# Kernel optimization log

Hardware: AMD Instinct MI355X
Metric: run time of the kernel (lower is better)

## Reference

```python
import jax, jax.numpy as jnp
import numpy as np

EPS_Q = 1e-5
EPS_RMS = 1e-6


def _bitlinear(x, w):
    # absmean ternary weight quantization with STE (STE irrelevant for fwd)
    w_scale = jnp.maximum(jnp.mean(jnp.abs(w)), EPS_Q)
    w_q = jnp.clip(jnp.round(w / w_scale), -1.0, 1.0)
    w_q = jax.lax.stop_gradient(w_q - w) + w
    # per-token absmax activation quantization
    x_scale = jnp.maximum(jnp.max(jnp.abs(x), axis=-1, keepdims=True), EPS_Q)
    x_s = x / x_scale
    out = jnp.einsum('bi,oi->bo', x_s, w_q)
    return out * x_scale


def _rmsnorm(x, g):
    rms = jnp.sqrt(jnp.mean(x * x, axis=-1, keepdims=True) + EPS_RMS)
    return x / rms * g


def setup_inputs() -> dict:
    key = jax.random.key(0)
    ks = jax.random.split(key, 6)
    B, IN, H, OUT = 65536, 784, 1024, 10
    return {
        'x': jax.random.normal(ks[0], (B, IN), dtype=jnp.float32),
        'w1': jax.random.normal(ks[1], (H, IN), dtype=jnp.float32) * 0.02,
        'g1': jnp.ones((H,), dtype=jnp.float32),
        'w2': jax.random.normal(ks[2], (H, H), dtype=jnp.float32) * 0.02,
        'g2': jnp.ones((H,), dtype=jnp.float32),
        'w3': jax.random.normal(ks[3], (OUT, H), dtype=jnp.float32) * 0.02,
    }


def reference(x, w1, g1, w2, g2, w3):
    h = _bitlinear(x, w1)
    h = jax.nn.gelu(_rmsnorm(h, g1), approximate=False)
    h = _bitlinear(h, w2)
    h = jax.nn.gelu(_rmsnorm(h, g2), approximate=False)
    return _bitlinear(h, w3)
```

## Files before the change

### kernel.cpp

```cpp
#include <hip/hip_runtime.h>
#include <hip/hip_bf16.h>
#include <stdint.h>


typedef __attribute__((ext_vector_type(8))) short short8;
typedef __attribute__((ext_vector_type(4))) float f32x4;

#define B_TOTAL 65536
#define IN_DIM 784
#define IN_PAD 832
#define H_DIM 1024
#define OUT_DIM 10
#define OUT_PAD 16

__device__ __forceinline__ unsigned short f2bf(float f) {
    union { float f; unsigned u; } c; c.f = f;
    unsigned r = c.u + 0x7FFFu + ((c.u >> 16) & 1u);
    return (unsigned short)(r >> 16);
}
__device__ __forceinline__ float bf2f(unsigned short h) {
    union { unsigned u; float f; } c; c.u = ((unsigned)h) << 16;
    return c.f;
}

__device__ __forceinline__ float gelu_fast(float t) {
    const float z = t * 0.70710678118f;
    const float s = fabsf(z);
    const float tt = 1.0f / (1.0f + 0.3275911f * s);
    const float e = __expf(-s * s);
    float p = fmaf(tt, 1.061405429f, -1.453152027f);
    p = fmaf(tt, p, 1.421413741f);
    p = fmaf(tt, p, -0.284496736f);
    p = fmaf(tt, p, 0.254829592f);
    float erfa = fmaf(-p * tt, e, 1.0f);
    erfa = copysignf(erfa, z);
    return 0.5f * t * (1.0f + erfa);
}

#define GLOAD16(gp, lp)                                                        \
    __builtin_amdgcn_global_load_lds(                                          \
        (const __attribute__((address_space(1))) void*)(gp),                   \
        (__attribute__((address_space(3))) void*)(lp), 16, 0, 0)

__global__ void absum3_kernel(const float* __restrict__ w1, const float* __restrict__ w2,
                              const float* __restrict__ w3, double* acc) {
    __shared__ float red[4];
    const int which = blockIdx.y;
    const float* w = (which == 0) ? w1 : (which == 1) ? w2 : w3;
    const int n = (which == 0) ? H_DIM * IN_DIM : (which == 1) ? H_DIM * H_DIM : OUT_DIM * H_DIM;
    float s = 0.f;
    for (int i = blockIdx.x * blockDim.x + threadIdx.x; i < n; i += gridDim.x * blockDim.x)
        s += fabsf(w[i]);
#pragma unroll
    for (int o = 32; o > 0; o >>= 1) s += __shfl_xor(s, o);
    if ((threadIdx.x & 63) == 0) red[threadIdx.x >> 6] = s;
    __syncthreads();
    if (threadIdx.x == 0) {
        float t = red[0] + red[1] + red[2] + red[3];
        atomicAdd(acc + which, (double)t);
    }
}

__global__ void quant_all(const float* __restrict__ w1, const float* __restrict__ w2,
                          const float* __restrict__ w3,
                          unsigned short* __restrict__ w1q, unsigned short* __restrict__ w2q,
                          unsigned short* __restrict__ w3q, const double* sums) {
    const int k = blockIdx.x * blockDim.x + threadIdx.x;
    const int y = blockIdx.y;
    const float* w; unsigned short* wq; int o, O, K, Kp, n; const double* sum;
    if (y < 1024)      { w = w1; wq = w1q; o = y;        O = H_DIM;  K = IN_DIM; Kp = IN_PAD; n = H_DIM * IN_DIM;  sum = sums + 0; }
    else if (y < 2048) { w = w2; wq = w2q; o = y - 1024; O = H_DIM;  K = H_DIM;  Kp = H_DIM;  n = H_DIM * H_DIM;  sum = sums + 1; }
    else               { w = w3; wq = w3q; o = y - 2048; O = OUT_DIM; K = H_DIM; Kp = H_DIM;  n = OUT_DIM * H_DIM; sum = sums + 2; }
    if (k >= Kp) return;
    float scale = fmaxf((float)(*sum / (double)n), 1e-5f);
    float q = 0.f;
    if (o < O && k < K) {
        float r = rintf(w[(size_t)o * K + k] / scale);
        q = fminf(1.f, fmaxf(-1.f, r));
    }
    wq[(size_t)o * Kp + k] = f2bf(q);
}

__global__ __launch_bounds__(256)
void convert_pad(const float* __restrict__ x, unsigned short* __restrict__ xb) {
    const int g = blockIdx.x * 256 + threadIdx.x;
    const int row = g / 104;
    const int c = (g % 104) * 8;
    short8 v = 0;
    if (c < IN_DIM) {
        const float* p = x + (size_t)row * IN_DIM + c;
        float4 f0 = *(const float4*)p;
        float4 f1 = *(const float4*)(p + 4);
        v[0] = (short)f2bf(f0.x); v[1] = (short)f2bf(f0.y);
        v[2] = (short)f2bf(f0.z); v[3] = (short)f2bf(f0.w);
        v[4] = (short)f2bf(f1.x); v[5] = (short)f2bf(f1.y);
        v[6] = (short)f2bf(f1.z); v[7] = (short)f2bf(f1.w);
    }
    *(short8*)(xb + (size_t)row * IN_PAD + c) = v;
}

template<int KP>
__global__ __launch_bounds__(512, 2)
void gemm_bt(const unsigned short* __restrict__ A, const unsigned short* __restrict__ Bq,
             unsigned short* __restrict__ C) {
    constexpr int NT = KP / 64;
    __shared__ __attribute__((aligned(16))) unsigned short LDS[65536];
    const int tid = threadIdx.x;
    const int lane = tid & 63;
    const int w = tid >> 6;
    const int wm = w >> 2, wn = w & 3;
    const int lr = lane & 15, gq = lane >> 4;
    const int gsw8 = (gq ^ ((lr >> 3) << 1)) * 8;
    const int lrO = lr * 32;
    const int bid = blockIdx.x;
    const int xcd = bid & 7, slot = bid >> 3;
    const int nblk = slot & 3;
    const int mblk = xcd * (gridDim.x >> 5) + (slot >> 2);
    const int m0 = mblk * 256, n0 = nblk * 256;
    const int rS = lane >> 2;
    const int cS = ((lane & 3) ^ ((lane >> 5) << 1)) * 8;
    const int stA0 = w;
    const int stA1 = 8 + w;
    const int stB_P1 = (w >> 2) * 8 + (w & 3);
    const int stB_P3 = stB_P1 + 4;

#define STG(gbase, areaS, st)                                                  \
    {   const unsigned short* _g = (gbase) +                                   \
            (size_t)(((st) >> 1) * 16 + rS) * KP + ((st) & 1) * 32 + cS;       \
        GLOAD16(_g, &LDS[(areaS) + (st) * 512]);                               \
        GLOAD16(_g + (size_t)128 * KP, &LDS[(areaS) + (st) * 512 + 8192]); }
#define RD_A(mq, mf, kk)                                                       \
    (*(const short8*)&LDS[curS + ((wm * 8 + (mq) * 4 + (mf)) * 2 + (kk)) * 512 + lrO + gsw8])
#define RD_B(nq, nf, kk)                                                       \
    (*(const short8*)&LDS[curS + 16384 + ((wn * 4 + (nq) * 2 + (nf)) * 2 + (kk)) * 512 + lrO + gsw8])
#define MM(mq, nq, mf, nf, kk)                                                 \
    acc[(mq) * 4 + (mf)][(nq) * 2 + (nf)] =                                    \
        __builtin_amdgcn_mfma_f32_16x16x32_bf16(af[mf][kk], bf[nf][kk],        \
            acc[(mq) * 4 + (mf)][(nq) * 2 + (nf)], 0, 0, 0)

    f32x4 acc[8][4] = {};
    short8 af[4][2], bf[2][2];
    STG(A + (size_t)m0 * KP, 0, stA0);
    STG(Bq + (size_t)n0 * KP, 16384, stB_P1);
    STG(Bq + (size_t)n0 * KP, 16384, stB_P3);
    STG(A + (size_t)m0 * KP, 0, stA1);
    STG(A + (size_t)m0 * KP + 64, 32768, stA0);
    STG(Bq + (size_t)n0 * KP + 64, 49152, stB_P3);
    STG(A + (size_t)m0 * KP + 64, 32768, stA1);
    asm volatile("s_waitcnt vmcnt(6)" ::: "memory");
#pragma unroll 2
    for (int t = 0; t < NT; ++t) {
        const int curS = (t & 1) * 32768;
        const int nxtS = curS ^ 32768;
        __builtin_amdgcn_s_barrier();
        af[0][0] = RD_A(0, 0, 0); bf[0][0] = RD_B(0, 0, 0);
        af[1][0] = RD_A(0, 1, 0); bf[1][0] = RD_B(0, 1, 0);
        __builtin_amdgcn_s_setprio(1);
        MM(0, 0, 0, 0, 0); af[2][0] = RD_A(0, 2, 0);
        MM(0, 0, 0, 1, 0); af[3][0] = RD_A(0, 3, 0);
        MM(0, 0, 1, 0, 0); af[0][1] = RD_A(0, 0, 1);
        MM(0, 0, 1, 1, 0); bf[0][1] = RD_B(0, 0, 1);
        MM(0, 0, 2, 0, 0); af[1][1] = RD_A(0, 1, 1);
        MM(0, 0, 2, 1, 0); bf[1][1] = RD_B(0, 1, 1);
        MM(0, 0, 3, 0, 0); af[2][1] = RD_A(0, 2, 1);
        MM(0, 0, 3, 1, 0); af[3][1] = RD_A(0, 3, 1);
        MM(0, 0, 0, 0, 1); bf[0][0] = RD_B(1, 0, 0);
        MM(0, 0, 0, 1, 1); bf[1][0] = RD_B(1, 1, 0);
        MM(0, 0, 1, 0, 1); MM(0, 0, 1, 1, 1);
        MM(0, 0, 2, 0, 1); MM(0, 0, 2, 1, 1);
        MM(0, 0, 3, 0, 1); MM(0, 0, 3, 1, 1);
        __builtin_amdgcn_s_setprio(0);
        bf[0][1] = RD_B(1, 0, 1); bf[1][1] = RD_B(1, 1, 1);
        if (t + 1 < NT) STG(Bq + (size_t)n0 * KP + (t + 1) * 64, nxtS + 16384, stB_P1);
        __builtin_amdgcn_s_barrier();
        __builtin_amdgcn_s_setprio(1);
        MM(0, 1, 0, 0, 0); MM(0, 1, 0, 1, 0); af[0][0] = RD_A(1, 0, 0);
        MM(0, 1, 1, 0, 0); MM(0, 1, 1, 1, 0); af[1][0] = RD_A(1, 1, 0);
        MM(0, 1, 2, 0, 0); MM(0, 1, 2, 1, 0); af[2][0] = RD_A(1, 2, 0);
        MM(0, 1, 3, 0, 0); MM(0, 1, 3, 1, 0); af[3][0] = RD_A(1, 3, 0);
        MM(0, 1, 0, 0, 1); MM(0, 1, 0, 1, 1); af[0][1] = RD_A(1, 0, 1);
        MM(0, 1, 1, 0, 1); MM(0, 1, 1, 1, 1); af[1][1] = RD_A(1, 1, 1);
        MM(0, 1, 2, 0, 1); MM(0, 1, 2, 1, 1); af[2][1] = RD_A(1, 2, 1);
        MM(0, 1, 3, 0, 1); MM(0, 1, 3, 1, 1); af[3][1] = RD_A(1, 3, 1);
        __builtin_amdgcn_s_setprio(0);
        if (t + 2 < NT) STG(A + (size_t)m0 * KP + (t + 2) * 64, curS, stA0);
        __builtin_amdgcn_s_barrier();
        __builtin_amdgcn_s_setprio(1);
        MM(1, 1, 0, 0, 0); MM(1, 1, 0, 1, 0);
        MM(1, 1, 1, 0, 0); MM(1, 1, 1, 1, 0);
        MM(1, 1, 2, 0, 0); MM(1, 1, 2, 1, 0);
        MM(1, 1, 3, 0, 0); MM(1, 1, 3, 1, 0);
        MM(1, 1, 0, 0, 1); bf[0][0] = RD_B(0, 0, 0);
        MM(1, 1, 0, 1, 1); bf[1][0] = RD_B(0, 1, 0);
        MM(1, 1, 1, 0, 1); MM(1, 1, 1, 1, 1);
        MM(1, 1, 2, 0, 1); MM(1, 1, 2, 1, 1);
        MM(1, 1, 3, 0, 1); MM(1, 1, 3, 1, 1);
        __builtin_amdgcn_s_setprio(0);
        bf[0][1] = RD_B(0, 0, 1); bf[1][1] = RD_B(0, 1, 1);
        if (t + 2 < NT) STG(Bq + (size_t)n0 * KP + (t + 2) * 64, curS + 16384, stB_P3);
        __builtin_amdgcn_s_barrier();
        __builtin_amdgcn_s_setprio(1);
        MM(1, 0, 0, 0, 0); MM(1, 0, 0, 1, 0);
        MM(1, 0, 1, 0, 0); MM(1, 0, 1, 1, 0);
        MM(1, 0, 2, 0, 0); MM(1, 0, 2, 1, 0);
        MM(1, 0, 3, 0, 0); MM(1, 0, 3, 1, 0);
        MM(1, 0, 0, 0, 1); MM(1, 0, 0, 1, 1);
        MM(1, 0, 1, 0, 1); MM(1, 0, 1, 1, 1);
        MM(1, 0, 2, 0, 1); MM(1, 0, 2, 1, 1);
        MM(1, 0, 3, 0, 1); MM(1, 0, 3, 1, 1);
        __builtin_amdgcn_s_setprio(0);
        if (t + 2 < NT) STG(A + (size_t)m0 * KP + (t + 2) * 64, curS, stA1);
        if (t < NT - 2) { asm volatile("s_waitcnt vmcnt(6)" ::: "memory"); }
        else            { asm volatile("s_waitcnt vmcnt(0)" ::: "memory"); }
    }
#pragma unroll
    for (int mf = 0; mf < 8; ++mf) {
        const int grow = m0 + wm * 128 + mf * 16 + (lane >> 4) * 4;
#pragma unroll
        for (int nf = 0; nf < 4; ++nf) {
            const int gcol = n0 + wn * 64 + nf * 16 + lr;
            unsigned short* Cp = C + (size_t)grow * H_DIM + gcol;
#pragma unroll
            for (int j = 0; j < 4; ++j) Cp[(size_t)j * H_DIM] = f2bf(acc[mf][nf][j]);
        }
    }
#undef STG
#undef RD_A
#undef RD_B
#undef MM
}

__global__ __launch_bounds__(256)
void norm_gelu(const unsigned short* __restrict__ Hp, const float* __restrict__ g,
               unsigned short* __restrict__ U) {
    const int row = blockIdx.x * 4 + (threadIdx.x >> 6);
    const int lane = threadIdx.x & 63;
    const unsigned short* rp = Hp + (size_t)row * H_DIM;
    short8 v0 = *(const short8*)(rp + lane * 8);
    short8 v1 = *(const short8*)(rp + 512 + lane * 8);
    float f[16];
#pragma unroll
    for (int j = 0; j < 8; ++j) {
        f[j] = bf2f((unsigned short)v0[j]);
        f[8 + j] = bf2f((unsigned short)v1[j]);
    }
    float s = 0.f;
#pragma unroll
    for (int j = 0; j < 16; ++j) s += f[j] * f[j];
#pragma unroll
    for (int o = 32; o > 0; o >>= 1) s += __shfl_xor(s, o);
    const float rinv = 1.f / sqrtf(s * (1.f / 1024.f) + 1e-6f);
    float4 ga0 = *(const float4*)(g + lane * 8);
    float4 ga1 = *(const float4*)(g + lane * 8 + 4);
    float4 gb0 = *(const float4*)(g + 512 + lane * 8);
    float4 gb1 = *(const float4*)(g + 512 + lane * 8 + 4);
    float gv[16] = {ga0.x, ga0.y, ga0.z, ga0.w, ga1.x, ga1.y, ga1.z, ga1.w,
                    gb0.x, gb0.y, gb0.z, gb0.w, gb1.x, gb1.y, gb1.z, gb1.w};
    short8 o0, o1;
#pragma unroll
    for (int j = 0; j < 8; ++j) {
        o0[j] = (short)f2bf(gelu_fast(f[j] * rinv * gv[j]));
        o1[j] = (short)f2bf(gelu_fast(f[8 + j] * rinv * gv[8 + j]));
    }
    unsigned short* up = U + (size_t)row * H_DIM;
    *(short8*)(up + lane * 8) = o0;
    *(short8*)(up + 512 + lane * 8) = o1;
}

__global__ __launch_bounds__(256)
void norm_gelu_out(const unsigned short* __restrict__ Hp, const float* __restrict__ g,
                   const unsigned short* __restrict__ w3q, float* __restrict__ out) {
    __shared__ unsigned short Us[16][1032];
    const int tid = threadIdx.x;
    const int lane = tid & 63, wid = tid >> 6;
    const size_t r0 = (size_t)blockIdx.x * 16;
    float4 ga0 = *(const float4*)(g + lane * 8);
    float4 ga1 = *(const float4*)(g + lane * 8 + 4);
    float4 gb0 = *(const float4*)(g + 512 + lane * 8);
    float4 gb1 = *(const float4*)(g + 512 + lane * 8 + 4);
    float gv[16] = {ga0.x, ga0.y, ga0.z, ga0.w, ga1.x, ga1.y, ga1.z, ga1.w,
                    gb0.x, gb0.y, gb0.z, gb0.w, gb1.x, gb1.y, gb1.z, gb1.w};
#pragma unroll
    for (int rr = 0; rr < 4; ++rr) {
        const int row = wid * 4 + rr;
        const unsigned short* rp = Hp + (r0 + row) * H_DIM;
        short8 v0 = *(const short8*)(rp + lane * 8);
        short8 v1 = *(const short8*)(rp + 512 + lane * 8);
        float f[16];
#pragma unroll
        for (int j = 0; j < 8; ++j) {
            f[j] = bf2f((unsigned short)v0[j]);
            f[8 + j] = bf2f((unsigned short)v1[j]);
        }
        float s = 0.f;
#pragma unroll
        for (int j = 0; j < 16; ++j) s += f[j] * f[j];
#pragma unroll
        for (int o = 32; o > 0; o >>= 1) s += __shfl_xor(s, o);
        const float rinv = 1.f / sqrtf(s * (1.f / 1024.f) + 1e-6f);
        short8 o0, o1;
#pragma unroll
        for (int j = 0; j < 8; ++j) {
            o0[j] = (short)f2bf(gelu_fast(f[j] * rinv * gv[j]));
            o1[j] = (short)f2bf(gelu_fast(f[8 + j] * rinv * gv[8 + j]));
        }
        *(short8*)&Us[row][lane * 8] = o0;
        *(short8*)&Us[row][512 + lane * 8] = o1;
    }
    __syncthreads();
    if (wid == 0) {
        const int lr = lane & 15, lk = (lane >> 4) * 8;
        f32x4 acc = {};
#pragma unroll 4
        for (int ks = 0; ks < 32; ++ks) {
            short8 a = *(const short8*)&Us[lr][ks * 32 + lk];
            short8 b = *(const short8*)(w3q + (size_t)lr * H_DIM + ks * 32 + lk);
            acc = __builtin_amdgcn_mfma_f32_16x16x32_bf16(a, b, acc, 0, 0, 0);
        }
        if (lr < OUT_DIM) {
#pragma unroll
            for (int j = 0; j < 4; ++j)
                out[(r0 + (lane >> 4) * 4 + j) * OUT_DIM + lr] = acc[j];
        }
    }
}

extern "C" void kernel_launch(void* const* d_in, const int* in_sizes, int n_in,
                              void* d_out, int out_size, void* d_ws, size_t ws_size,
                              hipStream_t stream) {
    (void)in_sizes; (void)n_in; (void)out_size;
    const float* x  = (const float*)d_in[0];
    const float* w1 = (const float*)d_in[1];
    const float* g1 = (const float*)d_in[2];
    const float* w2 = (const float*)d_in[3];
    const float* g2 = (const float*)d_in[4];
    const float* w3 = (const float*)d_in[5];
    float* out = (float*)d_out;

    uint8_t* ws = (uint8_t*)d_ws;
    double* sums = (double*)ws;
    size_t off = 256;
    unsigned short* w1q = (unsigned short*)(ws + off); off += (size_t)H_DIM * IN_PAD * 2;
    unsigned short* w2q = (unsigned short*)(ws + off); off += (size_t)H_DIM * H_DIM * 2;
    unsigned short* w3q = (unsigned short*)(ws + off); off += (size_t)OUT_PAD * H_DIM * 2;

    size_t rem = (ws_size > off) ? ws_size - off : 0;
    int R = B_TOTAL;
    while (R > 2048 && (size_t)2 * R * H_DIM * 2 > rem) R >>= 1;
    unsigned short* bufA = (unsigned short*)(ws + off);
    unsigned short* bufB = bufA + (size_t)R * H_DIM;

    hipMemsetAsync(sums, 0, 3 * sizeof(double), stream);
    absum3_kernel<<<dim3(128, 3), 256, 0, stream>>>(w1, w2, w3, sums);
    quant_all<<<dim3(4, 2064), 256, 0, stream>>>(w1, w2, w3, w1q, w2q, w3q, sums);

    const int nchunk = B_TOTAL / R;
    for (int c = 0; c < nchunk; ++c) {
        const float* xc = x + (size_t)c * R * IN_DIM;
        convert_pad<<<R * 104 / 256, 256, 0, stream>>>(xc, bufB);
        gemm_bt<IN_PAD><<<(R / 256) * 4, 512, 0, stream>>>(bufB, w1q, bufA);
        norm_gelu<<<R / 4, 256, 0, stream>>>(bufA, g1, bufB);
        gemm_bt<H_DIM><<<(R / 256) * 4, 512, 0, stream>>>(bufB, w2q, bufA);
        norm_gelu_out<<<R / 16, 256, 0, stream>>>(bufA, g2, w3q,
                                                  out + (size_t)c * R * OUT_DIM);
    }
}
```

Baseline: 439.1 us.

## Load GEMM B operand directly from global into registers, bypassing LDS

Weight (B) tiles are no longer staged through shared memory. Each wave now reads its B fragments straight from global memory into registers, one K-step ahead, and only the A tiles stay double-buffered in LDS. This halves the LDS footprint per block, which could allow two blocks per CU, and removes the B LDS stores and reads. The trade-off is extra global/L2 traffic, because waves re-fetch the same B rows. The loads have a strided access pattern with L2 latency exposed inside the MFMA loop, and the A pipeline wait (vmcnt) is tightened.

```diff
diff --git a/kernel.cpp b/kernel.cpp
--- a/kernel.cpp
+++ b/kernel.cpp
@@ -104,7 +104,7 @@
 void gemm_bt(const unsigned short* __restrict__ A, const unsigned short* __restrict__ Bq,
              unsigned short* __restrict__ C) {
     constexpr int NT = KP / 64;
-    __shared__ __attribute__((aligned(16))) unsigned short LDS[65536];
+    __shared__ __attribute__((aligned(16))) unsigned short LDS[32768];
     const int tid = threadIdx.x;
     const int lane = tid & 63;
     const int w = tid >> 6;
@@ -121,18 +121,20 @@
     const int cS = ((lane & 3) ^ ((lane >> 5) << 1)) * 8;
     const int stA0 = w;
     const int stA1 = 8 + w;
-    const int stB_P1 = (w >> 2) * 8 + (w & 3);
-    const int stB_P3 = stB_P1 + 4;
-
-#define STG(gbase, areaS, st)                                                  \
-    {   const unsigned short* _g = (gbase) +                                   \
-            (size_t)(((st) >> 1) * 16 + rS) * KP + ((st) & 1) * 32 + cS;       \
+    const unsigned short* bp[4];
+#pragma unroll
+    for (int i = 0; i < 4; ++i)
+        bp[i] = Bq + (size_t)(n0 + wn * 64 + i * 16 + lr) * KP + gq * 8;
+
+#define STG(tt, areaS, st)                                                     \
+    {   const unsigned short* _g = A +                                         \
+            (size_t)(m0 + ((st) >> 1) * 16 + rS) * KP + (tt) * 64 + ((st) & 1) * 32 + cS; \
         GLOAD16(_g, &LDS[(areaS) + (st) * 512]);                               \
         GLOAD16(_g + (size_t)128 * KP, &LDS[(areaS) + (st) * 512 + 8192]); }
 #define RD_A(mq, mf, kk)                                                       \
-    (*(const short8*)&LDS[curS + ((wm * 8 + (mq) * 4 + (mf)) * 2 + (kk)) * 512 + lrO + gsw8])
-#define RD_B(nq, nf, kk)                                                       \
-    (*(const short8*)&LDS[curS + 16384 + ((wn * 4 + (nq) * 2 + (nf)) * 2 + (kk)) * 512 + lrO + gsw8])
+    (*(const short8*)&LDS[curA + ((wm * 8 + (mq) * 4 + (mf)) * 2 + (kk)) * 512 + lrO + gsw8])
+#define GB(nq, nf, kk, tt)                                                     \
+    (*(const short8*)(bp[(nq) * 2 + (nf)] + (tt) * 64 + (kk) * 32))
 #define MM(mq, nq, mf, nf, kk)                                                 \
     acc[(mq) * 4 + (mf)][(nq) * 2 + (nf)] =                                    \
         __builtin_amdgcn_mfma_f32_16x16x32_bf16(af[mf][kk], bf[nf][kk],        \
@@ -140,38 +142,33 @@
 
     f32x4 acc[8][4] = {};
     short8 af[4][2], bf[2][2];
-    STG(A + (size_t)m0 * KP, 0, stA0);
-    STG(Bq + (size_t)n0 * KP, 16384, stB_P1);
-    STG(Bq + (size_t)n0 * KP, 16384, stB_P3);
-    STG(A + (size_t)m0 * KP, 0, stA1);
-    STG(A + (size_t)m0 * KP + 64, 32768, stA0);
-    STG(Bq + (size_t)n0 * KP + 64, 49152, stB_P3);
-    STG(A + (size_t)m0 * KP + 64, 32768, stA1);
-    asm volatile("s_waitcnt vmcnt(6)" ::: "memory");
+    STG(0, 0, stA0); STG(0, 0, stA1);
+    asm volatile("s_waitcnt vmcnt(0)" ::: "memory");
+    STG(1, 16384, stA0); STG(1, 16384, stA1);
+    bf[0][0] = GB(0, 0, 0, 0); bf[1][0] = GB(0, 1, 0, 0);
+    bf[0][1] = GB(0, 0, 1, 0); bf[1][1] = GB(0, 1, 1, 0);
 #pragma unroll 2
     for (int t = 0; t < NT; ++t) {
-        const int curS = (t & 1) * 32768;
-        const int nxtS = curS ^ 32768;
+        const int curA = (t & 1) * 16384;
         __builtin_amdgcn_s_barrier();
-        af[0][0] = RD_A(0, 0, 0); bf[0][0] = RD_B(0, 0, 0);
-        af[1][0] = RD_A(0, 1, 0); bf[1][0] = RD_B(0, 1, 0);
+        af[0][0] = RD_A(0, 0, 0);
+        af[1][0] = RD_A(0, 1, 0);
         __builtin_amdgcn_s_setprio(1);
         MM(0, 0, 0, 0, 0); af[2][0] = RD_A(0, 2, 0);
         MM(0, 0, 0, 1, 0); af[3][0] = RD_A(0, 3, 0);
         MM(0, 0, 1, 0, 0); af[0][1] = RD_A(0, 0, 1);
-        MM(0, 0, 1, 1, 0); bf[0][1] = RD_B(0, 0, 1);
-        MM(0, 0, 2, 0, 0); af[1][1] = RD_A(0, 1, 1);
-        MM(0, 0, 2, 1, 0); bf[1][1] = RD_B(0, 1, 1);
-        MM(0, 0, 3, 0, 0); af[2][1] = RD_A(0, 2, 1);
-        MM(0, 0, 3, 1, 0); af[3][1] = RD_A(0, 3, 1);
-        MM(0, 0, 0, 0, 1); bf[0][0] = RD_B(1, 0, 0);
-        MM(0, 0, 0, 1, 1); bf[1][0] = RD_B(1, 1, 0);
+        MM(0, 0, 1, 1, 0); af[1][1] = RD_A(0, 1, 1);
+        MM(0, 0, 2, 0, 0); af[2][1] = RD_A(0, 2, 1);
+        MM(0, 0, 2, 1, 0); af[3][1] = RD_A(0, 3, 1);
+        MM(0, 0, 3, 0, 0);
+        MM(0, 0, 3, 1, 0);
+        MM(0, 0, 0, 0, 1); bf[0][0] = GB(1, 0, 0, t);
+        MM(0, 0, 0, 1, 1); bf[1][0] = GB(1, 1, 0, t);
         MM(0, 0, 1, 0, 1); MM(0, 0, 1, 1, 1);
         MM(0, 0, 2, 0, 1); MM(0, 0, 2, 1, 1);
         MM(0, 0, 3, 0, 1); MM(0, 0, 3, 1, 1);
         __builtin_amdgcn_s_setprio(0);
-        bf[0][1] = RD_B(1, 0, 1); bf[1][1] = RD_B(1, 1, 1);
-        if (t + 1 < NT) STG(Bq + (size_t)n0 * KP + (t + 1) * 64, nxtS + 16384, stB_P1);
+        bf[0][1] = GB(1, 0, 1, t); bf[1][1] = GB(1, 1, 1, t);
         __builtin_amdgcn_s_barrier();
         __builtin_amdgcn_s_setprio(1);
         MM(0, 1, 0, 0, 0); MM(0, 1, 0, 1, 0); af[0][0] = RD_A(1, 0, 0);
@@ -183,21 +180,20 @@
         MM(0, 1, 2, 0, 1); MM(0, 1, 2, 1, 1); af[2][1] = RD_A(1, 2, 1);
         MM(0, 1, 3, 0, 1); MM(0, 1, 3, 1, 1); af[3][1] = RD_A(1, 3, 1);
         __builtin_amdgcn_s_setprio(0);
-        if (t + 2 < NT) STG(A + (size_t)m0 * KP + (t + 2) * 64, curS, stA0);
+        if (t + 2 < NT) STG(t + 2, curA, stA0);
         __builtin_amdgcn_s_barrier();
         __builtin_amdgcn_s_setprio(1);
         MM(1, 1, 0, 0, 0); MM(1, 1, 0, 1, 0);
         MM(1, 1, 1, 0, 0); MM(1, 1, 1, 1, 0);
         MM(1, 1, 2, 0, 0); MM(1, 1, 2, 1, 0);
         MM(1, 1, 3, 0, 0); MM(1, 1, 3, 1, 0);
-        MM(1, 1, 0, 0, 1); bf[0][0] = RD_B(0, 0, 0);
-        MM(1, 1, 0, 1, 1); bf[1][0] = RD_B(0, 1, 0);
+        MM(1, 1, 0, 0, 1); bf[0][0] = GB(0, 0, 0, t);
+        MM(1, 1, 0, 1, 1); bf[1][0] = GB(0, 1, 0, t);
         MM(1, 1, 1, 0, 1); MM(1, 1, 1, 1, 1);
         MM(1, 1, 2, 0, 1); MM(1, 1, 2, 1, 1);
         MM(1, 1, 3, 0, 1); MM(1, 1, 3, 1, 1);
         __builtin_amdgcn_s_setprio(0);
-        bf[0][1] = RD_B(0, 0, 1); bf[1][1] = RD_B(0, 1, 1);
-        if (t + 2 < NT) STG(Bq + (size_t)n0 * KP + (t + 2) * 64, curS + 16384, stB_P3);
+        bf[0][1] = GB(0, 0, 1, t); bf[1][1] = GB(0, 1, 1, t);
         __builtin_amdgcn_s_barrier();
         __builtin_amdgcn_s_setprio(1);
         MM(1, 0, 0, 0, 0); MM(1, 0, 0, 1, 0);
@@ -209,8 +205,12 @@
         MM(1, 0, 2, 0, 1); MM(1, 0, 2, 1, 1);
         MM(1, 0, 3, 0, 1); MM(1, 0, 3, 1, 1);
         __builtin_amdgcn_s_setprio(0);
-        if (t + 2 < NT) STG(A + (size_t)m0 * KP + (t + 2) * 64, curS, stA1);
-        if (t < NT - 2) { asm volatile("s_waitcnt vmcnt(6)" ::: "memory"); }
+        if (t + 2 < NT) STG(t + 2, curA, stA1);
+        if (t + 1 < NT) {
+            bf[0][0] = GB(0, 0, 0, t + 1); bf[1][0] = GB(0, 1, 0, t + 1);
+            bf[0][1] = GB(0, 0, 1, t + 1); bf[1][1] = GB(0, 1, 1, t + 1);
+        }
+        if (t < NT - 2) { asm volatile("s_waitcnt vmcnt(4)" ::: "memory"); }
         else            { asm volatile("s_waitcnt vmcnt(0)" ::: "memory"); }
     }
 #pragma unroll
@@ -226,7 +226,7 @@
     }
 #undef STG
 #undef RD_A
-#undef RD_B
+#undef GB
 #undef MM
 }
 
```

Measured after the change: 587.5 us. 33.8% more time.
